# Optimization experiments

Hardware: AMD Instinct MI355X
Metric: run time of the kernel (lower is better)

## Reference

```python
import jax, jax.numpy as jnp
import numpy as np

N_USERS, N_ITEMS = 100000, 200000
D, L, N_L = 256, 16, 3
B, T, N_TGT = 512, 16, 32


def setup_inputs() -> dict:
    key = jax.random.key(0)
    ks = jax.random.split(key, 12)
    seq_var = jax.random.randint(ks[0], (B, T), 0, N_ITEMS)
    user_var = jax.random.randint(ks[1], (B,), 0, N_USERS)
    item_var = jax.random.randint(ks[2], (B, N_TGT), 0, N_ITEMS)
    item_emb = jax.random.normal(ks[3], (N_ITEMS, D), jnp.float32) / D
    user_emb = jax.random.normal(ks[4], (N_USERS, D), jnp.float32) / D
    # conv_w[l, m, c, d_in]: kernel for length-(l+1) conv; tap m = lag m (m=0 is current step).
    # taps m>l are structurally zero (emulates the L separate Conv2d(1, d, (l+1, d)) kernels).
    scale = 1.0 / np.sqrt(L * D)
    conv_w = jax.random.normal(ks[5], (L, L, D, D), jnp.float32) * scale
    tap_mask = (jnp.arange(L)[None, :] <= jnp.arange(L)[:, None]).astype(jnp.float32)  # [L, L]
    conv_w = conv_w * tap_mask[:, :, None, None]
    conv_b = jax.random.normal(ks[6], (L, D), jnp.float32) * scale
    fc1_w = jax.random.normal(ks[7], (D, 2 * D), jnp.float32) / np.sqrt(2 * D)
    fc1_b = jax.random.normal(ks[8], (D,), jnp.float32) / np.sqrt(2 * D)
    W2 = jax.random.normal(ks[9], (N_ITEMS, D), jnp.float32) / D
    b2 = jnp.zeros((N_ITEMS, 1), jnp.float32)
    return {"seq_var": seq_var, "user_var": user_var, "item_var": item_var,
            "item_emb": item_emb, "user_emb": user_emb, "conv_w": conv_w,
            "conv_b": conv_b, "fc1_w": fc1_w, "fc1_b": fc1_b, "W2": W2, "b2": b2}


def _forget_mult(f, x):
    # QRNN fo-pooling: h_t = f_t * x_t + (1 - f_t) * h_{t-1}, h_0 = 0. f, x: [T, B, D]
    def step(h, fx):
        ft, xt = fx
        hn = ft * xt + (1.0 - ft) * h
        return hn, hn
    _, hs = jax.lax.scan(step, jnp.zeros_like(x[0]), (f, x))
    return hs  # [T, B, D]


def reference(seq_var, user_var, item_var, item_emb, user_emb, conv_w, conv_b, fc1_w, fc1_b, W2, b2):
    emb = item_emb[seq_var]                      # [B, T, D]
    Lk = conv_w.shape[0]
    padded = jnp.pad(emb, ((0, 0), (Lk - 1, 0), (0, 0)))
    # windows X[b, t, m, :] = emb[b, t - m, :] (zero for t - m < 0)
    X = jnp.stack([padded[:, Lk - 1 - m: Lk - 1 - m + emb.shape[1], :] for m in range(Lk)], axis=2)  # [B,T,L,D]
    conv_out = jnp.einsum('btmd,lmcd->lbtc', X, conv_w) + conv_b[:, None, None, :]  # [L,B,T,D]
    f = jax.nn.sigmoid(jax.nn.relu(conv_out))    # ac_conv=relu then sigmoid gate
    f = jnp.transpose(f, (0, 2, 1, 3))           # [L, T, B, D]
    x0 = jnp.transpose(emb, (1, 0, 2))           # [T, B, D]

    def chain(f_l):
        x = x0
        for _ in range(N_L):
            x = _forget_mult(f_l, x)
        return x                                  # [T, B, D]

    h = jax.vmap(chain)(f)                       # [L, T, B, D]
    o = h.sum(axis=(0, 1))                       # [B, D] (sum over T per conv, accumulated over L)
    cat = jnp.concatenate([o, user_emb[user_var]], axis=1)   # [B, 2D]; dropout p=0 -> identity
    z = cat @ fc1_w.T + fc1_b                    # [B, D]
    w2 = W2[item_var]                            # [B, N_TGT, D]
    b2v = b2[item_var][..., 0]                   # [B, N_TGT]
    res = jnp.einsum('bnd,bd->bn', w2, z) + b2v  # baddbmm train branch
    return res
```

## Files before the change

kernel.cpp:

```cpp
#include <hip/hip_runtime.h>

typedef __bf16 bf16x8 __attribute__((ext_vector_type(8)));
typedef float  floatx4 __attribute__((ext_vector_type(4)));

__device__ __forceinline__ unsigned short f2b(float f) {
  union { float f; unsigned int u; } v; v.f = f;
  unsigned int r = v.u + 0x7FFFu + ((v.u >> 16) & 1u);
  return (unsigned short)(r >> 16);
}
__device__ __forceinline__ float b2f(unsigned short h) {
  union { unsigned int u; float f; } v; v.u = ((unsigned int)h) << 16;
  return v.f;
}
__device__ __forceinline__ void gld16(const void* g, void* l) {
  __builtin_amdgcn_global_load_lds(
      (const __attribute__((address_space(1))) unsigned int*)g,
      (__attribute__((address_space(3))) unsigned int*)l, 16, 0, 0);
}

__global__ __launch_bounds__(256) void cvt_w_kernel(const float* __restrict__ w,
                                                    unsigned short* __restrict__ wr) {
  int gid = blockIdx.x * 256 + threadIdx.x;
  int dc = gid & 31;
  int c  = (gid >> 5) & 255;
  int m  = (gid >> 13) & 15;
  int l  = gid >> 17;
  if (m > l) return;
  const float4* src = (const float4*)(w + (size_t)gid * 8);
  float4 v0 = src[0], v1 = src[1];
  ushort4 h0, h1;
  h0.x = f2b(v0.x); h0.y = f2b(v0.y); h0.z = f2b(v0.z); h0.w = f2b(v0.w);
  h1.x = f2b(v1.x); h1.y = f2b(v1.y); h1.z = f2b(v1.z); h1.w = f2b(v1.w);
  int hh = c >> 7, cl = c & 127;
  int kt = m * 4 + (dc >> 3);
  int phys = (dc & 7) ^ (cl & 7);
  size_t off = (((size_t)(l * 2 + hh) * 64 + (size_t)kt) * 128 + cl) * 64 + phys * 8;
  *(ushort4*)(wr + off)     = h0;
  *(ushort4*)(wr + off + 4) = h1;
}

__global__ __launch_bounds__(64) void gather_kernel(const int* __restrict__ seq,
                                                    const float* __restrict__ item_emb,
                                                    float* __restrict__ ef,
                                                    unsigned short* __restrict__ eb) {
  int row = blockIdx.x;
  int c4  = threadIdx.x;
  int t   = row & 15;
  int idx = seq[row];
  float4 v = ((const float4*)(item_emb + (size_t)idx * 256))[c4];
  ((float4*)(ef + (size_t)row * 256))[c4] = v;
  ushort4 h; h.x = f2b(v.x); h.y = f2b(v.y); h.z = f2b(v.z); h.w = f2b(v.w);
  int j = c4 >> 1, half = c4 & 1;
  int pp = (((j ^ (t & 7)) & 7) | (j & 24)) * 2 + half;
  ((ushort4*)(eb + (size_t)row * 256))[pp] = h;
}

__global__ __launch_bounds__(256, 4) void conv_qrnn_kernel(
    const unsigned short* __restrict__ Abf,
    const unsigned short* __restrict__ Wr,
    const float* __restrict__ embf,
    const float* __restrict__ conv_b,
    const char* __restrict__ zp,
    float* __restrict__ o)
{
  __shared__ union {
    struct { unsigned short A[128 * 64]; unsigned short B[128 * 64]; } st;
    unsigned short fT[128 * 128];
  } sm;

  const int tid  = threadIdx.x;
  const int lane = tid & 63;
  const int wave = tid >> 6;
  const int wm   = wave >> 1;
  const int wn   = wave & 1;
  const int lrow = lane & 15;
  const int kq   = lane >> 4;

  const int bid = blockIdx.x;
  const int l   = 15 - (bid >> 7);
  const int sub = bid & 127;
  const int bm  = sub >> 1;
  const int c0  = (sub & 1) << 7;

  const int tA = (tid >> 3) & 15;
  const int bh = tid >> 7;
  const int ck = tid & 7;
  const char* const AbfB = (const char*)Abf;
  const size_t gb0 = ((size_t)(bm * 8 + bh) * 16 + tA) * 512 + (size_t)ck * 16;
  const char* const WrB = (const char*)Wr + (size_t)((l * 2) + (sub & 1)) * 64 * 16384;

  floatx4 acc[4][4];
  #pragma unroll
  for (int i = 0; i < 4; ++i)
    #pragma unroll
    for (int j = 0; j < 4; ++j)
      acc[i][j] = floatx4{0.f, 0.f, 0.f, 0.f};

  for (int m = 0; m <= l; ++m) {
    const char* srcA[4];
    {
      const bool valid = (tA >= m);
      const size_t base = gb0 - (size_t)m * 512;
      #pragma unroll
      for (int it = 0; it < 4; ++it)
        srcA[it] = valid ? (AbfB + base + (size_t)it * 16384) : (zp + ck * 16);
    }
    const int swzA = (lrow - m) & 7;
    for (int db = 0; db < 4; ++db) {
      const int kt = m * 4 + db;
      #pragma unroll
      for (int it = 0; it < 4; ++it)
        gld16(srcA[it] + db * 128, (char*)sm.st.A + ((size_t)(it * 256 + tid)) * 16);
      const char* wsrc = WrB + (size_t)kt * 16384;
      #pragma unroll
      for (int it = 0; it < 4; ++it)
        gld16(wsrc + (size_t)(it * 256 + tid) * 16, (char*)sm.st.B + ((size_t)(it * 256 + tid)) * 16);
      __syncthreads();
      #pragma unroll
      for (int ks = 0; ks < 2; ++ks) {
        const int pa = (((ks * 4 + kq) ^ swzA) & 7) * 8;
        const int pb = (((ks * 4 + kq) ^ lrow) & 7) * 8;
        bf16x8 aF[4], bF[4];
        #pragma unroll
        for (int i = 0; i < 4; ++i)
          aF[i] = *(const bf16x8*)&sm.st.A[(wm * 64 + i * 16 + lrow) * 64 + pa];
        #pragma unroll
        for (int j = 0; j < 4; ++j)
          bF[j] = *(const bf16x8*)&sm.st.B[(wn * 64 + j * 16 + lrow) * 64 + pb];
        #pragma unroll
        for (int i = 0; i < 4; ++i)
          #pragma unroll
          for (int j = 0; j < 4; ++j)
            acc[i][j] = __builtin_amdgcn_mfma_f32_16x16x32_bf16(aF[i], bF[j], acc[i][j], 0, 0, 0);
      }
      __syncthreads();
    }
  }

  #pragma unroll
  for (int j = 0; j < 4; ++j) {
    int col = wn * 64 + j * 16 + lrow;
    float cb = conv_b[l * 256 + c0 + col];
    #pragma unroll
    for (int i = 0; i < 4; ++i) {
      #pragma unroll
      for (int r = 0; r < 4; ++r) {
        int row = wm * 64 + i * 16 + kq * 4 + r;
        float x = acc[i][j][r] + cb;
        x = fmaxf(x, 0.f);
        float f = 1.f / (1.f + __expf(-x));
        sm.fT[row * 128 + col] = f2b(f);
      }
    }
  }
  __syncthreads();

  #pragma unroll
  for (int q = 0; q < 4; ++q) {
    int p   = q * 256 + tid;
    int c_l = p & 127;
    int b_l = p >> 7;
    int b_g = bm * 8 + b_l;
    int c   = c0 + c_l;
    float xv[16], fv[16];
    #pragma unroll
    for (int t = 0; t < 16; ++t) {
      xv[t] = embf[((size_t)b_g * 16 + t) * 256 + c];
      fv[t] = b2f(sm.fT[(b_l * 16 + t) * 128 + c_l]);
    }
    #pragma unroll
    for (int pass = 0; pass < 3; ++pass) {
      float h = 0.f;
      #pragma unroll
      for (int t = 0; t < 16; ++t) { h = fv[t] * xv[t] + (1.f - fv[t]) * h; xv[t] = h; }
    }
    float s = 0.f;
    #pragma unroll
    for (int t = 0; t < 16; ++t) s += xv[t];
    atomicAdd(&o[b_g * 256 + c], s);
  }
}

__global__ __launch_bounds__(256) void head_kernel(
    const float* __restrict__ o, const float* __restrict__ user_emb,
    const int* __restrict__ user_var, const float* __restrict__ fc1_w,
    const float* __restrict__ fc1_b, const float* __restrict__ W2,
    const float* __restrict__ b2, const int* __restrict__ item_var,
    float* __restrict__ out)
{
  __shared__ __align__(16) float cat[512];
  __shared__ __align__(16) float zz[256];
  int b = blockIdx.x;
  int tid = threadIdx.x;
  int uid = user_var[b];
  cat[tid]       = o[b * 256 + tid];
  cat[256 + tid] = user_emb[(size_t)uid * 256 + tid];
  __syncthreads();
  float a = fc1_b[tid];
  const float4* wr = (const float4*)(fc1_w + tid * 512);
  #pragma unroll 4
  for (int k4 = 0; k4 < 128; ++k4) {
    float4 w4 = wr[k4];
    a += w4.x * cat[k4 * 4] + w4.y * cat[k4 * 4 + 1] + w4.z * cat[k4 * 4 + 2] + w4.w * cat[k4 * 4 + 3];
  }
  zz[tid] = a;
  __syncthreads();
  int n = tid >> 3, s = tid & 7;
  int it = item_var[b * 32 + n];
  const float4* w   = (const float4*)(W2 + (size_t)it * 256);
  const float4* zv4 = (const float4*)zz;
  float acc = 0.f;
  #pragma unroll
  for (int i = 0; i < 8; ++i) {
    int k4 = i * 8 + s;
    float4 wv = w[k4];
    float4 zv = zv4[k4];
    acc += wv.x * zv.x + wv.y * zv.y + wv.z * zv.z + wv.w * zv.w;
  }
  acc += __shfl_down(acc, 4, 8);
  acc += __shfl_down(acc, 2, 8);
  acc += __shfl_down(acc, 1, 8);
  if (s == 0) out[b * 32 + n] = acc + b2[it];
}

extern "C" void kernel_launch(void* const* d_in, const int* in_sizes, int n_in,
                              void* d_out, int out_size, void* d_ws, size_t ws_size,
                              hipStream_t stream) {
  (void)in_sizes; (void)n_in; (void)out_size; (void)ws_size;
  const int*   seq_var  = (const int*)d_in[0];
  const int*   user_var = (const int*)d_in[1];
  const int*   item_var = (const int*)d_in[2];
  const float* item_emb = (const float*)d_in[3];
  const float* user_emb = (const float*)d_in[4];
  const float* conv_w   = (const float*)d_in[5];
  const float* conv_b   = (const float*)d_in[6];
  const float* fc1_w    = (const float*)d_in[7];
  const float* fc1_b    = (const float*)d_in[8];
  const float* W2       = (const float*)d_in[9];
  const float* b2       = (const float*)d_in[10];
  float* out = (float*)d_out;

  char* ws = (char*)d_ws;
  unsigned short* cwr = (unsigned short*)ws;
  unsigned short* ebf = (unsigned short*)(ws + 33554432);
  float*          ef  = (float*)(ws + 33554432 + 4194304);
  float*          o   = (float*)(ws + 33554432 + 4194304 + 8388608);
  char*           zp  = ws + 33554432 + 4194304 + 8388608 + 524288;

  hipMemsetAsync(o, 0, 524288 + 512, stream);
  cvt_w_kernel<<<8192, 256, 0, stream>>>(conv_w, cwr);
  gather_kernel<<<8192, 64, 0, stream>>>(seq_var, item_emb, ef, ebf);
  conv_qrnn_kernel<<<2048, 256, 0, stream>>>(ebf, cwr, ef, conv_b, zp, o);
  head_kernel<<<512, 256, 0, stream>>>(o, user_emb, user_var, fc1_w, fc1_b, W2, b2, item_var, out);
}
```

Baseline: 597.4 us.

## Widen conv tile to full 256 channels, merge prep kernels, transpose fc1 weights

The conv+QRNN kernel now computes all 256 output channels per block (128x256 tile, 8 B fragments per wave) instead of splitting channels across two blocks. This halves the grid and removes the duplicated A-tile loads, at the cost of doubled accumulator registers and LDS, with occupancy lowered to 2. The weight conversion, embedding gather, and a new fc1_w transpose are merged into one prep launch. The head kernel reads the transposed fc1 weights so its loads are coalesced across threads.

```diff
diff --git a/kernel.cpp b/kernel.cpp
--- a/kernel.cpp
+++ b/kernel.cpp
@@ -18,44 +18,64 @@
       (__attribute__((address_space(3))) unsigned int*)l, 16, 0, 0);
 }
 
-__global__ __launch_bounds__(256) void cvt_w_kernel(const float* __restrict__ w,
-                                                    unsigned short* __restrict__ wr) {
-  int gid = blockIdx.x * 256 + threadIdx.x;
-  int dc = gid & 31;
-  int c  = (gid >> 5) & 255;
-  int m  = (gid >> 13) & 15;
-  int l  = gid >> 17;
-  if (m > l) return;
-  const float4* src = (const float4*)(w + (size_t)gid * 8);
-  float4 v0 = src[0], v1 = src[1];
-  ushort4 h0, h1;
-  h0.x = f2b(v0.x); h0.y = f2b(v0.y); h0.z = f2b(v0.z); h0.w = f2b(v0.w);
-  h1.x = f2b(v1.x); h1.y = f2b(v1.y); h1.z = f2b(v1.z); h1.w = f2b(v1.w);
-  int hh = c >> 7, cl = c & 127;
-  int kt = m * 4 + (dc >> 3);
-  int phys = (dc & 7) ^ (cl & 7);
-  size_t off = (((size_t)(l * 2 + hh) * 64 + (size_t)kt) * 128 + cl) * 64 + phys * 8;
-  *(ushort4*)(wr + off)     = h0;
-  *(ushort4*)(wr + off + 4) = h1;
-}
-
-__global__ __launch_bounds__(64) void gather_kernel(const int* __restrict__ seq,
-                                                    const float* __restrict__ item_emb,
-                                                    float* __restrict__ ef,
-                                                    unsigned short* __restrict__ eb) {
-  int row = blockIdx.x;
-  int c4  = threadIdx.x;
-  int t   = row & 15;
-  int idx = seq[row];
-  float4 v = ((const float4*)(item_emb + (size_t)idx * 256))[c4];
-  ((float4*)(ef + (size_t)row * 256))[c4] = v;
-  ushort4 h; h.x = f2b(v.x); h.y = f2b(v.y); h.z = f2b(v.z); h.w = f2b(v.w);
-  int j = c4 >> 1, half = c4 & 1;
-  int pp = (((j ^ (t & 7)) & 7) | (j & 24)) * 2 + half;
-  ((ushort4*)(eb + (size_t)row * 256))[pp] = h;
-}
-
-__global__ __launch_bounds__(256, 4) void conv_qrnn_kernel(
+__global__ __launch_bounds__(256) void prep_kernel(
+    const float* __restrict__ w, unsigned short* __restrict__ wr,
+    const int* __restrict__ seq, const float* __restrict__ item_emb,
+    float* __restrict__ ef, unsigned short* __restrict__ eb,
+    const float* __restrict__ fc1_w, float* __restrict__ fwT)
+{
+  __shared__ float tl[64][65];
+  const int bid = blockIdx.x, tid = threadIdx.x;
+  if (bid < 8192) {
+    int gid = bid * 256 + tid;
+    int dc = gid & 31;
+    int c  = (gid >> 5) & 255;
+    int m  = (gid >> 13) & 15;
+    int l  = gid >> 17;
+    if (m > l) return;
+    const float4* src = (const float4*)(w + (size_t)gid * 8);
+    float4 v0 = src[0], v1 = src[1];
+    ushort4 h0, h1;
+    h0.x = f2b(v0.x); h0.y = f2b(v0.y); h0.z = f2b(v0.z); h0.w = f2b(v0.w);
+    h1.x = f2b(v1.x); h1.y = f2b(v1.y); h1.z = f2b(v1.z); h1.w = f2b(v1.w);
+    int kt = m * 4 + (dc >> 3);
+    int phys = (dc & 7) ^ (c & 7);
+    size_t off = (((size_t)(l * 64 + kt)) * 256 + c) * 64 + phys * 8;
+    *(ushort4*)(wr + off)     = h0;
+    *(ushort4*)(wr + off + 4) = h1;
+  } else if (bid < 10240) {
+    int row = (bid - 8192) * 4 + (tid >> 6);
+    int c4  = tid & 63;
+    int t   = row & 15;
+    int idx = seq[row];
+    float4 v = ((const float4*)(item_emb + (size_t)idx * 256))[c4];
+    ((float4*)(ef + (size_t)row * 256))[c4] = v;
+    ushort4 h; h.x = f2b(v.x); h.y = f2b(v.y); h.z = f2b(v.z); h.w = f2b(v.w);
+    int j = c4 >> 1, half = c4 & 1;
+    int pp = (((j ^ (t & 7)) & 7) | (j & 24)) * 2 + half;
+    ((ushort4*)(eb + (size_t)row * 256))[pp] = h;
+  } else {
+    int tb = bid - 10240;
+    int j0 = (tb >> 3) * 64, k0 = (tb & 7) * 64;
+    #pragma unroll
+    for (int it = 0; it < 4; ++it) {
+      int q = it * 256 + tid, j = q >> 4, k4 = q & 15;
+      float4 v = *(const float4*)(fc1_w + (size_t)(j0 + j) * 512 + k0 + k4 * 4);
+      tl[j][k4 * 4 + 0] = v.x; tl[j][k4 * 4 + 1] = v.y;
+      tl[j][k4 * 4 + 2] = v.z; tl[j][k4 * 4 + 3] = v.w;
+    }
+    __syncthreads();
+    #pragma unroll
+    for (int it = 0; it < 4; ++it) {
+      int q = it * 256 + tid, k = q >> 4, j4 = q & 15;
+      float4 v = { tl[j4 * 4 + 0][k], tl[j4 * 4 + 1][k],
+                   tl[j4 * 4 + 2][k], tl[j4 * 4 + 3][k] };
+      *(float4*)(fwT + (size_t)(k0 + k) * 256 + j0 + j4 * 4) = v;
+    }
+  }
+}
+
+__global__ __launch_bounds__(256, 2) void conv_qrnn_kernel(
     const unsigned short* __restrict__ Abf,
     const unsigned short* __restrict__ Wr,
     const float* __restrict__ embf,
@@ -64,8 +84,8 @@
     float* __restrict__ o)
 {
   __shared__ union {
-    struct { unsigned short A[128 * 64]; unsigned short B[128 * 64]; } st;
-    unsigned short fT[128 * 128];
+    struct { unsigned short A[128 * 64]; unsigned short B[256 * 64]; } st;
+    unsigned short fT[128 * 256];
   } sm;
 
   const int tid  = threadIdx.x;
@@ -77,23 +97,21 @@
   const int kq   = lane >> 4;
 
   const int bid = blockIdx.x;
-  const int l   = 15 - (bid >> 7);
-  const int sub = bid & 127;
-  const int bm  = sub >> 1;
-  const int c0  = (sub & 1) << 7;
+  const int l   = 15 - (bid >> 6);
+  const int bm  = bid & 63;
 
   const int tA = (tid >> 3) & 15;
   const int bh = tid >> 7;
   const int ck = tid & 7;
   const char* const AbfB = (const char*)Abf;
   const size_t gb0 = ((size_t)(bm * 8 + bh) * 16 + tA) * 512 + (size_t)ck * 16;
-  const char* const WrB = (const char*)Wr + (size_t)((l * 2) + (sub & 1)) * 64 * 16384;
-
-  floatx4 acc[4][4];
+  const char* const WrB = (const char*)Wr + (size_t)l * 64 * 32768;
+
+  floatx4 acc[4][8];
   #pragma unroll
   for (int i = 0; i < 4; ++i)
     #pragma unroll
-    for (int j = 0; j < 4; ++j)
+    for (int j = 0; j < 8; ++j)
       acc[i][j] = floatx4{0.f, 0.f, 0.f, 0.f};
 
   for (int m = 0; m <= l; ++m) {
@@ -111,26 +129,26 @@
       #pragma unroll
       for (int it = 0; it < 4; ++it)
         gld16(srcA[it] + db * 128, (char*)sm.st.A + ((size_t)(it * 256 + tid)) * 16);
-      const char* wsrc = WrB + (size_t)kt * 16384;
-      #pragma unroll
-      for (int it = 0; it < 4; ++it)
+      const char* wsrc = WrB + (size_t)kt * 32768;
+      #pragma unroll
+      for (int it = 0; it < 8; ++it)
         gld16(wsrc + (size_t)(it * 256 + tid) * 16, (char*)sm.st.B + ((size_t)(it * 256 + tid)) * 16);
       __syncthreads();
       #pragma unroll
       for (int ks = 0; ks < 2; ++ks) {
         const int pa = (((ks * 4 + kq) ^ swzA) & 7) * 8;
         const int pb = (((ks * 4 + kq) ^ lrow) & 7) * 8;
-        bf16x8 aF[4], bF[4];
+        bf16x8 aF[4], bF[8];
         #pragma unroll
         for (int i = 0; i < 4; ++i)
           aF[i] = *(const bf16x8*)&sm.st.A[(wm * 64 + i * 16 + lrow) * 64 + pa];
         #pragma unroll
-        for (int j = 0; j < 4; ++j)
-          bF[j] = *(const bf16x8*)&sm.st.B[(wn * 64 + j * 16 + lrow) * 64 + pb];
+        for (int j = 0; j < 8; ++j)
+          bF[j] = *(const bf16x8*)&sm.st.B[(wn * 128 + j * 16 + lrow) * 64 + pb];
         #pragma unroll
         for (int i = 0; i < 4; ++i)
           #pragma unroll
-          for (int j = 0; j < 4; ++j)
+          for (int j = 0; j < 8; ++j)
             acc[i][j] = __builtin_amdgcn_mfma_f32_16x16x32_bf16(aF[i], bF[j], acc[i][j], 0, 0, 0);
       }
       __syncthreads();
@@ -138,9 +156,9 @@
   }
 
   #pragma unroll
-  for (int j = 0; j < 4; ++j) {
-    int col = wn * 64 + j * 16 + lrow;
-    float cb = conv_b[l * 256 + c0 + col];
+  for (int j = 0; j < 8; ++j) {
+    int col = wn * 128 + j * 16 + lrow;
+    float cb = conv_b[l * 256 + col];
     #pragma unroll
     for (int i = 0; i < 4; ++i) {
       #pragma unroll
@@ -149,24 +167,23 @@
         float x = acc[i][j][r] + cb;
         x = fmaxf(x, 0.f);
         float f = 1.f / (1.f + __expf(-x));
-        sm.fT[row * 128 + col] = f2b(f);
+        sm.fT[row * 256 + col] = f2b(f);
       }
     }
   }
   __syncthreads();
 
   #pragma unroll
-  for (int q = 0; q < 4; ++q) {
+  for (int q = 0; q < 8; ++q) {
     int p   = q * 256 + tid;
-    int c_l = p & 127;
-    int b_l = p >> 7;
+    int c   = p & 255;
+    int b_l = p >> 8;
     int b_g = bm * 8 + b_l;
-    int c   = c0 + c_l;
     float xv[16], fv[16];
     #pragma unroll
     for (int t = 0; t < 16; ++t) {
       xv[t] = embf[((size_t)b_g * 16 + t) * 256 + c];
-      fv[t] = b2f(sm.fT[(b_l * 16 + t) * 128 + c_l]);
+      fv[t] = b2f(sm.fT[(b_l * 16 + t) * 256 + c]);
     }
     #pragma unroll
     for (int pass = 0; pass < 3; ++pass) {
@@ -183,7 +200,7 @@
 
 __global__ __launch_bounds__(256) void head_kernel(
     const float* __restrict__ o, const float* __restrict__ user_emb,
-    const int* __restrict__ user_var, const float* __restrict__ fc1_w,
+    const int* __restrict__ user_var, const float* __restrict__ fwT,
     const float* __restrict__ fc1_b, const float* __restrict__ W2,
     const float* __restrict__ b2, const int* __restrict__ item_var,
     float* __restrict__ out)
@@ -197,12 +214,9 @@
   cat[256 + tid] = user_emb[(size_t)uid * 256 + tid];
   __syncthreads();
   float a = fc1_b[tid];
-  const float4* wr = (const float4*)(fc1_w + tid * 512);
-  #pragma unroll 4
-  for (int k4 = 0; k4 < 128; ++k4) {
-    float4 w4 = wr[k4];
-    a += w4.x * cat[k4 * 4] + w4.y * cat[k4 * 4 + 1] + w4.z * cat[k4 * 4 + 2] + w4.w * cat[k4 * 4 + 3];
-  }
+  #pragma unroll 8
+  for (int k = 0; k < 512; ++k)
+    a += fwT[(size_t)k * 256 + tid] * cat[k];
   zz[tid] = a;
   __syncthreads();
   int n = tid >> 3, s = tid & 7;
@@ -243,13 +257,13 @@
   char* ws = (char*)d_ws;
   unsigned short* cwr = (unsigned short*)ws;
   unsigned short* ebf = (unsigned short*)(ws + 33554432);
-  float*          ef  = (float*)(ws + 33554432 + 4194304);
-  float*          o   = (float*)(ws + 33554432 + 4194304 + 8388608);
-  char*           zp  = ws + 33554432 + 4194304 + 8388608 + 524288;
+  float*          ef  = (float*)(ws + 37748736);
+  float*          o   = (float*)(ws + 46137344);
+  char*           zp  = ws + 46661632;
+  float*          fwT = (float*)(ws + 46662144);
 
   hipMemsetAsync(o, 0, 524288 + 512, stream);
-  cvt_w_kernel<<<8192, 256, 0, stream>>>(conv_w, cwr);
-  gather_kernel<<<8192, 64, 0, stream>>>(seq_var, item_emb, ef, ebf);
-  conv_qrnn_kernel<<<2048, 256, 0, stream>>>(ebf, cwr, ef, conv_b, zp, o);
-  head_kernel<<<512, 256, 0, stream>>>(o, user_emb, user_var, fc1_w, fc1_b, W2, b2, item_var, out);
-}
+  prep_kernel<<<10272, 256, 0, stream>>>(conv_w, cwr, seq_var, item_emb, ef, ebf, fc1_w, fwT);
+  conv_qrnn_kernel<<<1024, 256, 0, stream>>>(ebf, cwr, ef, conv_b, zp, o);
+  head_kernel<<<512, 256, 0, stream>>>(o, user_emb, user_var, fwT, fc1_b, W2, b2, item_var, out);
+}
```

Measured after the change: 569.1 us. 4.7% less time.
